# Optimization experiments

Measured on AMD Instinct MI355X. Metric: run time of the kernel, lower is better.

The kernel has to match this reference:

```python
import jax, jax.numpy as jnp
import numpy as np

T, B, A, H = 128, 32, 6, 128  # rollout len, envs, actions, lstm hidden


def _conv(x, w, b, stride):
    # x: NCHW, w: OIHW (torch layout), VALID padding like nn.Conv2d default
    y = jax.lax.conv_general_dilated(
        x, w, (stride, stride), 'VALID',
        dimension_numbers=('NCHW', 'OIHW', 'NCHW'))
    return y + b[None, :, None, None]


def setup_inputs() -> dict:
    key = jax.random.key(0)
    ks = jax.random.split(key, 12)
    s = 0.05  # weight scale to keep activations in a sane range
    inp = {
        'x': jax.random.uniform(ks[0], (T * B, 1, 84, 84), jnp.float32) * 255.0,
        'done': (jax.random.uniform(ks[1], (T * B,)) < 0.05).astype(jnp.float32),
        'h0': jnp.zeros((1, B, H), jnp.float32),
        'c0': jnp.zeros((1, B, H), jnp.float32),
        'W1': jax.random.normal(ks[2], (32, 1, 8, 8), jnp.float32) * s,
        'b1': jnp.zeros((32,), jnp.float32),
        'W2': jax.random.normal(ks[3], (64, 32, 4, 4), jnp.float32) * s,
        'b2': jnp.zeros((64,), jnp.float32),
        'W3': jax.random.normal(ks[4], (64, 64, 3, 3), jnp.float32) * s,
        'b3': jnp.zeros((64,), jnp.float32),
        'Wfc': jax.random.normal(ks[5], (512, 3136), jnp.float32) * s,
        'bfc': jnp.zeros((512,), jnp.float32),
        'W_ih': jax.random.normal(ks[6], (4 * H, 512), jnp.float32) * s,
        'W_hh': jax.random.normal(ks[7], (4 * H, H), jnp.float32) * s,
        'b_ih': jnp.zeros((4 * H,), jnp.float32),
        'b_hh': jnp.zeros((4 * H,), jnp.float32),
        'Wa': jax.random.normal(ks[8], (A, H), jnp.float32) * 0.01,
        'ba': jnp.zeros((A,), jnp.float32),
        'Wc': jax.random.normal(ks[9], (1, H), jnp.float32) * s,
        'bc': jnp.zeros((1,), jnp.float32),
    }
    return inp


def reference(x, done, h0, c0, W1, b1, W2, b2, W3, b3, Wfc, bfc,
              W_ih, W_hh, b_ih, b_hh, Wa, ba, Wc, bc):
    # --- conv feature extractor (x / 255.0) ---
    z = x / 255.0
    z = jax.nn.relu(_conv(z, W1, b1, 4))   # (N,32,20,20)
    z = jax.nn.relu(_conv(z, W2, b2, 2))   # (N,64,9,9)
    z = jax.nn.relu(_conv(z, W3, b3, 1))   # (N,64,7,7)
    z = z.reshape(z.shape[0], -1)           # (N,3136), torch flatten order
    hidden = jax.nn.relu(z @ Wfc.T + bfc)   # (N,512)

    batch = h0.shape[1]
    xs = hidden.reshape(-1, batch, 512)     # (T,B,512)
    ds = done.reshape(-1, batch)            # (T,B)

    # precompute input projection for all steps at once
    gates_x = jnp.einsum('tbi,gi->tbg', xs, W_ih) + b_ih  # (T,B,4H)

    def step(carry, inp):
        h, c = carry
        gx, d = inp
        mask = (1.0 - d)[:, None]           # reset state where done
        h = h * mask
        c = c * mask
        gates = gx + h @ W_hh.T + b_hh
        i, f, g, o = jnp.split(gates, 4, axis=-1)  # torch gate order i,f,g,o
        c = jax.nn.sigmoid(f) * c + jax.nn.sigmoid(i) * jnp.tanh(g)
        h = jax.nn.sigmoid(o) * jnp.tanh(c)
        return (h, c), h

    (hT, cT), hs = jax.lax.scan(step, (h0[0], c0[0]), (gates_x, ds))
    new_hidden = hs.reshape(-1, hs.shape[-1])  # (T*B, 128)

    logits = new_hidden @ Wa.T + ba            # (T*B, A)
    value = new_hidden @ Wc.T + bc             # (T*B, 1)
    return logits, value, hT[None], cT[None]
```

## Files before the change

kernel.cpp:

```cpp
#include <hip/hip_runtime.h>

#define TT 128
#define BB 32
#define NN (TT*BB)

typedef float f4 __attribute__((ext_vector_type(4)));
typedef float f32x4 __attribute__((ext_vector_type(4)));
typedef short s8 __attribute__((ext_vector_type(8)));
typedef short bf16x8 __attribute__((ext_vector_type(8)));
typedef short s4v __attribute__((ext_vector_type(4)));

__device__ __forceinline__ float bf2f(unsigned short u){
  union{unsigned int i; float f;} x; x.i = ((unsigned int)u)<<16; return x.f;
}
__device__ __forceinline__ unsigned short f2bf(float f){
  union{float ff; unsigned int i;} x; x.ff=f;
  unsigned int r = x.i + 0x7FFFu + ((x.i>>16)&1u);
  return (unsigned short)(r>>16);
}
__device__ __forceinline__ float fsig(float x){
  return __builtin_amdgcn_rcpf(1.f + __expf(-x));
}
__device__ __forceinline__ float ftanh(float x){
  return 1.f - 2.f*__builtin_amdgcn_rcpf(1.f + __expf(2.f*x));
}
__device__ __forceinline__ void gload_lds16(const void* g, void* lds){
  __builtin_amdgcn_global_load_lds(
    (const __attribute__((address_space(1))) unsigned int*)g,
    (__attribute__((address_space(3))) unsigned int*)lds, 16, 0, 0);
}

__global__ __launch_bounds__(256) void prep_w1(const float* __restrict__ W1,
    unsigned short* __restrict__ w1c){
  int i = blockIdx.x*256 + threadIdx.x;
  int co = i >> 6; int k = i & 63;
  w1c[i] = (co < 32) ? f2bf(W1[co*64 + k] * (1.f/255.f)) : (unsigned short)0;
}
__global__ __launch_bounds__(256) void prep_w2(const float* __restrict__ W2,
    unsigned short* __restrict__ w2c){
  int i = blockIdx.x*256 + threadIdx.x;
  int co = i >> 9; int rem = i & 511; int khw = rem >> 5; int ci = rem & 31;
  w2c[i] = f2bf(W2[(co*32 + ci)*16 + khw]);
}
__global__ __launch_bounds__(256) void prep_w3(const float* __restrict__ W3,
    unsigned short* __restrict__ w3c){
  int i = blockIdx.x*256 + threadIdx.x;
  int co = i/576; int rem = i - co*576; int khw = rem >> 6; int ci = rem & 63;
  w3c[i] = f2bf(W3[(co*64 + ci)*9 + khw]);
}
__global__ __launch_bounds__(256) void prep_wfc(const float* __restrict__ Wfc,
    unsigned short* __restrict__ wfcc){
  int i = blockIdx.x*256 + threadIdx.x;
  int nn = i/3136; int rem = i - nn*3136; int sp = rem >> 6; int ci = rem & 63;
  wfcc[i] = f2bf(Wfc[nn*3136 + ci*49 + sp]);
}
__global__ __launch_bounds__(256) void prep_wih(const float* __restrict__ W_ih,
    unsigned short* __restrict__ wihc){
  int i = blockIdx.x*256 + threadIdx.x;
  wihc[i] = f2bf(W_ih[i]);
}
__global__ __launch_bounds__(256) void prep_whh(const float* __restrict__ W_hh,
    unsigned short* __restrict__ whhc){
  int i = blockIdx.x*256 + threadIdx.x;
  whhc[i] = f2bf(W_hh[i]);
}
__global__ __launch_bounds__(256) void prep_x(const float* __restrict__ x,
    unsigned short* __restrict__ xb){
  int i = blockIdx.x*256 + threadIdx.x;
  f4 v0 = *(const f4*)(x + (size_t)i*8);
  f4 v1 = *(const f4*)(x + (size_t)i*8 + 4);
  s8 o;
  #pragma unroll
  for(int j=0;j<4;j++){ o[j] = (short)f2bf(v0[j]); o[4+j] = (short)f2bf(v1[j]); }
  *(s8*)&xb[(size_t)i*8] = o;
}

template<int MODE, int OUTBF16, int RELU>
__global__ __launch_bounds__(256) void mgemm_k(
    const unsigned short* __restrict__ A, const unsigned short* __restrict__ B,
    const float* __restrict__ bias1, const float* __restrict__ bias2,
    void* __restrict__ Cout, int K, int Nld, int nout){
  __shared__ unsigned short As[128*40];
  __shared__ unsigned short Bs[64*40];
  int t = threadIdx.x;
  int bm = blockIdx.y, bn = blockIdx.x;
  int arow = t >> 1, ahalf = t & 1;
  int gm = bm*128 + arow;
  const unsigned short* abase;
  if(MODE == 0){
    abase = A + (size_t)gm*K + ahalf*16;
  } else if(MODE == 1){
    int n = gm/81; int r = gm - n*81; int oh = r/9; int ow = r - oh*9;
    abase = A + (((size_t)n*20 + 2*oh)*20 + 2*ow)*32 + ahalf*16;
  } else if(MODE == 2){
    int n = gm/49; int r = gm - n*49; int oh = r/7; int ow = r - oh*7;
    abase = A + (((size_t)n*9 + oh)*9 + ow)*64 + ahalf*16;
  } else {
    int n = gm/400; int r = gm - n*400; int oh = r/20; int ow = r - oh*20;
    abase = A + (size_t)n*7056 + (size_t)(oh*4)*84 + ow*4;
  }
  int brow = t >> 2, bq = t & 3;
  const unsigned short* bbase = B + (size_t)(bn*64 + brow)*K + bq*8;
  int l = t & 63, w = t >> 6;
  int wr = w >> 1, wc = w & 1;
  int lr = l & 15, lk = (l >> 4)*8;
  f32x4 acc[4][2] = {};
  int nsteps = K >> 5;
  for(int s=0; s<nsteps; s++){
    if(MODE == 3){
      const unsigned short* src = abase + (size_t)(s*4 + ahalf*2)*84;
      s4v p0 = *(const s4v*)src;
      s4v p1 = *(const s4v*)(src + 4);
      s4v p2 = *(const s4v*)(src + 84);
      s4v p3 = *(const s4v*)(src + 88);
      *(s4v*)&As[arow*40 + ahalf*16]      = p0;
      *(s4v*)&As[arow*40 + ahalf*16 + 4]  = p1;
      *(s4v*)&As[arow*40 + ahalf*16 + 8]  = p2;
      *(s4v*)&As[arow*40 + ahalf*16 + 12] = p3;
    } else {
      const unsigned short* src;
      if(MODE == 0){
        src = abase + s*32;
      } else if(MODE == 1){
        int kh = s >> 2, kw = s & 3;
        src = abase + (kh*20 + kw)*32;
      } else {
        int khw = s >> 1; int kh = khw/3; int kw = khw - kh*3;
        src = abase + (kh*9 + kw)*64 + (s & 1)*32;
      }
      bf16x8 a0 = *(const bf16x8*)src;
      bf16x8 a1 = *(const bf16x8*)(src + 8);
      *(bf16x8*)&As[arow*40 + ahalf*16] = a0;
      *(bf16x8*)&As[arow*40 + ahalf*16 + 8] = a1;
    }
    bf16x8 bv = *(const bf16x8*)(bbase + s*32);
    *(bf16x8*)&Bs[brow*40 + bq*8] = bv;
    __syncthreads();
    bf16x8 af[4];
    #pragma unroll
    for(int mf=0; mf<4; mf++)
      af[mf] = *(const bf16x8*)&As[(wr*64 + mf*16 + lr)*40 + lk];
    bf16x8 b0 = *(const bf16x8*)&Bs[(wc*32 + lr)*40 + lk];
    bf16x8 b1 = *(const bf16x8*)&Bs[(wc*32 + 16 + lr)*40 + lk];
    #pragma unroll
    for(int mf=0; mf<4; mf++){
      acc[mf][0] = __builtin_amdgcn_mfma_f32_16x16x32_bf16(af[mf], b0, acc[mf][0], 0, 0, 0);
      acc[mf][1] = __builtin_amdgcn_mfma_f32_16x16x32_bf16(af[mf], b1, acc[mf][1], 0, 0, 0);
    }
    __syncthreads();
  }
  #pragma unroll
  for(int nf=0; nf<2; nf++){
    int gcol = bn*64 + wc*32 + nf*16 + lr;
    if(gcol >= nout) continue;
    float bb = bias1[gcol] + (bias2 ? bias2[gcol] : 0.f);
    #pragma unroll
    for(int mf=0; mf<4; mf++){
      #pragma unroll
      for(int reg=0; reg<4; reg++){
        int grow = bm*128 + wr*64 + mf*16 + (l>>4)*4 + reg;
        float v = acc[mf][nf][reg] + bb;
        if(RELU) v = v>0.f ? v : 0.f;
        if(OUTBF16) ((unsigned short*)Cout)[(size_t)grow*Nld + gcol] = f2bf(v);
        else        ((float*)Cout)[(size_t)grow*Nld + gcol] = v;
      }
    }
  }
}

__global__ __launch_bounds__(512) void lstm_v3_k(
    const float* __restrict__ gx,
    const float* __restrict__ done,
    const float* __restrict__ h0, const float* __restrict__ c0,
    const unsigned short* __restrict__ whhc,
    float* __restrict__ hs, float* __restrict__ out_hT, float* __restrict__ out_cT){
  __shared__ float mask_lds[TT*4];
  __shared__ unsigned short hA[2][4][136];
  __shared__ __align__(16) float gxS[3][4][520];
  __shared__ __align__(16) float gW[8][256];
  int tid = threadIdx.x;
  int B0 = blockIdx.x * 4;
  int w = tid >> 6, l = tid & 63;
  int lr = l & 15, lg = l >> 4;
  int cu = 16*w + (l >> 2);
  int cb = l & 3;
  int drow = w >> 1, dhalf = w & 1;

  bf16x8 wA[4][4];
  #pragma unroll
  for(int g=0; g<4; g++)
    #pragma unroll
    for(int kt=0; kt<4; kt++)
      wA[g][kt] = *(const bf16x8*)&whhc[(size_t)(g*128 + 16*w + lr)*128 + kt*32 + lg*8];

  {
    int tt = tid >> 2, bb = tid & 3;
    mask_lds[tid] = 1.f - done[tt*32 + B0 + bb];
  }
  float cv = c0[(size_t)(B0+cb)*128 + cu];
  float hv0 = h0[(size_t)(B0+cb)*128 + cu];
  float hout = 0.f;
  {
    float m0 = 1.f - done[0*BB + B0 + cb];
    hA[0][cb][cu] = f2bf(hv0 * m0);
  }
  #pragma unroll
  for(int sl=0; sl<2; sl++)
    gload_lds16(gx + ((size_t)(sl*32 + B0 + drow))*512 + dhalf*256 + l*4,
                &gxS[sl][drow][dhalf*256]);
  __syncthreads();

  int slot = 0;
  for(int t=0; t<TT; t++){
    int cur = t & 1;
    {
      int ts = (t+2 < TT) ? t+2 : TT-1;
      int s2 = (slot >= 1) ? slot-1 : 2;
      gload_lds16(gx + ((size_t)(ts*32 + B0 + drow))*512 + dhalf*256 + l*4,
                  &gxS[s2][drow][dhalf*256]);
    }
    bf16x8 hF[4];
    #pragma unroll
    for(int kt=0; kt<4; kt++)
      hF[kt] = *(const bf16x8*)&hA[cur][lr & 3][kt*32 + lg*8];
    f32x4 acc[4] = {};
    #pragma unroll
    for(int kt=0; kt<4; kt++)
      #pragma unroll
      for(int g=0; g<4; g++)
        acc[g] = __builtin_amdgcn_mfma_f32_16x16x32_bf16(wA[g][kt], hF[kt], acc[g], 0, 0, 0);
    if(lr < 4){
      #pragma unroll
      for(int g=0; g<4; g++)
        #pragma unroll
        for(int r=0; r<4; r++)
          gW[w][(lg*4 + r)*16 + lr*4 + g] = acc[g][r];
    }
    asm volatile("s_waitcnt lgkmcnt(0)" ::: "memory");
    f4 g4 = *(const f4*)&gW[w][l*4];
    float gx0 = gxS[slot][cb][      cu];
    float gx1 = gxS[slot][cb][128 + cu];
    float gx2 = gxS[slot][cb][256 + cu];
    float gx3 = gxS[slot][cb][384 + cu];
    float m  = mask_lds[t*4 + cb];
    float mn = (t < TT-1) ? mask_lds[(t+1)*4 + cb] : 1.f;
    float iv = fsig (g4[0] + gx0);
    float fv = fsig (g4[1] + gx1);
    float gv = ftanh(g4[2] + gx2);
    float ov = fsig (g4[3] + gx3);
    float cn = fv*(cv*m) + iv*gv;
    float hn = ov*ftanh(cn);
    cv = cn; hout = hn;
    hs[((size_t)t*BB + B0 + cb)*128 + cu] = hn;
    hA[cur^1][cb][cu] = f2bf(hn * mn);
    asm volatile("s_waitcnt vmcnt(3) lgkmcnt(0)" ::: "memory");
    __builtin_amdgcn_s_barrier();
    slot = (slot >= 2) ? 0 : slot+1;
  }
  out_hT[(size_t)(B0+cb)*128 + cu] = hout;
  out_cT[(size_t)(B0+cb)*128 + cu] = cv;
}

__global__ __launch_bounds__(256) void heads_k(const float* __restrict__ hs,
    const float* __restrict__ Wa, const float* __restrict__ ba,
    const float* __restrict__ Wc, const float* __restrict__ bc,
    float* __restrict__ out){
  int gid = blockIdx.x*256 + threadIdx.x;
  int n = gid/7, a = gid - n*7;
  const float* w = (a<6) ? (Wa + a*128) : Wc;
  float bias = (a<6) ? ba[a] : bc[0];
  const float* h = hs + (size_t)n*128;
  float acc = 0.f;
  #pragma unroll
  for(int k=0;k<32;k++){
    f4 hv = *(const f4*)(h + k*4);
    f4 wv = *(const f4*)(w + k*4);
    acc += hv[0]*wv[0]+hv[1]*wv[1]+hv[2]*wv[2]+hv[3]*wv[3];
  }
  float v = acc + bias;
  if(a<6) out[(size_t)n*6 + a] = v;
  else    out[24576 + n] = v;
}

extern "C" void kernel_launch(void* const* d_in, const int* in_sizes, int n_in,
                              void* d_out, int out_size, void* d_ws, size_t ws_size,
                              hipStream_t stream){
  const float* x    = (const float*)d_in[0];
  const float* done = (const float*)d_in[1];
  const float* h0   = (const float*)d_in[2];
  const float* c0   = (const float*)d_in[3];
  const float* W1   = (const float*)d_in[4];
  const float* b1   = (const float*)d_in[5];
  const float* W2   = (const float*)d_in[6];
  const float* b2   = (const float*)d_in[7];
  const float* W3   = (const float*)d_in[8];
  const float* b3   = (const float*)d_in[9];
  const float* Wfc  = (const float*)d_in[10];
  const float* bfc  = (const float*)d_in[11];
  const float* W_ih = (const float*)d_in[12];
  const float* W_hh = (const float*)d_in[13];
  const float* b_ih = (const float*)d_in[14];
  const float* b_hh = (const float*)d_in[15];
  const float* Wa   = (const float*)d_in[16];
  const float* ba   = (const float*)d_in[17];
  const float* Wc   = (const float*)d_in[18];
  const float* bc   = (const float*)d_in[19];
  float* out = (float*)d_out;

  char* ws = (char*)d_ws;
  unsigned short* z1   = (unsigned short*)(ws + 0);
  unsigned short* xb16 = (unsigned short*)(ws + 104857600);
  unsigned short* z2   = (unsigned short*)(ws + 104857600);
  unsigned short* z3   = (unsigned short*)(ws + 0);
  unsigned short* hid  = (unsigned short*)(ws + 25690112);
  float* gx            = (float*)(ws + 29884416);
  float* hs            = (float*)(ws + 38273024);
  unsigned short* w2c  = (unsigned short*)(ws + 162660352);
  unsigned short* w3c  = (unsigned short*)(ws + 162725888);
  unsigned short* wfcc = (unsigned short*)(ws + 162799616);
  unsigned short* wihc = (unsigned short*)(ws + 166010880);
  unsigned short* w1c  = (unsigned short*)(ws + 166535168);
  unsigned short* whhc = (unsigned short*)(ws + 166543360);

  prep_w1 <<<16,  256, 0, stream>>>(W1, w1c);
  prep_w2 <<<128, 256, 0, stream>>>(W2, w2c);
  prep_w3 <<<144, 256, 0, stream>>>(W3, w3c);
  prep_wfc<<<6272,256, 0, stream>>>(Wfc, wfcc);
  prep_wih<<<1024,256, 0, stream>>>(W_ih, wihc);
  prep_whh<<<256, 256, 0, stream>>>(W_hh, whhc);
  prep_x  <<<14112,256,0, stream>>>(x, xb16);

  mgemm_k<3,1,1><<<dim3(1,12800),256,0,stream>>>(xb16, w1c, b1, nullptr, z1, 64, 32, 32);
  mgemm_k<1,1,1><<<dim3(1,2592),256,0,stream>>>(z1, w2c, b2, nullptr, z2, 512, 64, 64);
  mgemm_k<2,1,1><<<dim3(1,1568),256,0,stream>>>(z2, w3c, b3, nullptr, z3, 576, 64, 64);
  mgemm_k<0,1,1><<<dim3(8,32),256,0,stream>>>(z3, wfcc, bfc, nullptr, hid, 3136, 512, 512);
  mgemm_k<0,0,0><<<dim3(8,32),256,0,stream>>>(hid, wihc, b_ih, b_hh, gx, 512, 512, 512);

  lstm_v3_k<<<8,512,0,stream>>>(gx, done, h0, c0, whhc, hs, out+28672, out+32768);
  heads_k<<<112,256,0,stream>>>(hs, Wa, ba, Wc, bc, out);
}
```

Before: 360.2 us.

## Fuse input conversion, conv1 and conv2 into one per-image LDS kernel

Adds a per-image kernel that loads the fp32 frame, converts it to bf16 in LDS, runs conv1 with MFMA into an LDS buffer, then runs conv2 from LDS and writes only z2. This drops the bf16 copy of x, the global z1 round trip and two launches. The conv3 GEMM also gets a block-index swizzle, and the LSTM gate scratch layout changes to scalar reads. One block per image uses a lot of LDS, which can limit occupancy.

```diff
diff --git a/kernel.cpp b/kernel.cpp
--- a/kernel.cpp
+++ b/kernel.cpp
@@ -33,8 +33,7 @@
 __global__ __launch_bounds__(256) void prep_w1(const float* __restrict__ W1,
     unsigned short* __restrict__ w1c){
   int i = blockIdx.x*256 + threadIdx.x;
-  int co = i >> 6; int k = i & 63;
-  w1c[i] = (co < 32) ? f2bf(W1[co*64 + k] * (1.f/255.f)) : (unsigned short)0;
+  w1c[i] = f2bf(W1[i] * (1.f/255.f));
 }
 __global__ __launch_bounds__(256) void prep_w2(const float* __restrict__ W2,
     unsigned short* __restrict__ w2c){
@@ -64,18 +63,114 @@
   int i = blockIdx.x*256 + threadIdx.x;
   whhc[i] = f2bf(W_hh[i]);
 }
-__global__ __launch_bounds__(256) void prep_x(const float* __restrict__ x,
-    unsigned short* __restrict__ xb){
-  int i = blockIdx.x*256 + threadIdx.x;
-  f4 v0 = *(const f4*)(x + (size_t)i*8);
-  f4 v1 = *(const f4*)(x + (size_t)i*8 + 4);
-  s8 o;
-  #pragma unroll
-  for(int j=0;j<4;j++){ o[j] = (short)f2bf(v0[j]); o[4+j] = (short)f2bf(v1[j]); }
-  *(s8*)&xb[(size_t)i*8] = o;
-}
-
-template<int MODE, int OUTBF16, int RELU>
+
+__global__ __launch_bounds__(256) void conv12_k(
+    const float* __restrict__ x,
+    const unsigned short* __restrict__ w1c, const float* __restrict__ b1,
+    const unsigned short* __restrict__ w2c, const float* __restrict__ b2,
+    unsigned short* __restrict__ z2){
+  __shared__ unsigned short xI[84*88];
+  __shared__ unsigned short z1[400*34];
+  __shared__ unsigned short w1L[32*68];
+  __shared__ unsigned short w2L[64*520];
+  int t = threadIdx.x;
+  int n = blockIdx.x;
+  int w = t >> 6, l = t & 63;
+  int lr = l & 15, lg = l >> 4;
+
+  {
+    bf16x8 v = *(const bf16x8*)&w1c[t*8];
+    *(bf16x8*)&w1L[(t>>3)*68 + (t&7)*8] = v;
+  }
+  {
+    int row = t >> 2, c0 = (t & 3)*128;
+    #pragma unroll
+    for(int j=0;j<16;j++){
+      bf16x8 v = *(const bf16x8*)&w2c[row*512 + c0 + j*8];
+      *(bf16x8*)&w2L[row*520 + c0 + j*8] = v;
+    }
+  }
+  {
+    const float* xb = x + (size_t)n*7056;
+    #pragma unroll
+    for(int j=0;j<7;j++){
+      int idx = t + 256*j;
+      if(idx < 1764){
+        f4 v = *(const f4*)(xb + idx*4);
+        s4v p;
+        #pragma unroll
+        for(int e=0;e<4;e++) p[e] = (short)f2bf(v[e]);
+        int row = idx/21, col = (idx - row*21)*4;
+        *(s4v*)&xI[row*88 + col] = p;
+      }
+    }
+  }
+  __syncthreads();
+
+  bf16x8 bf1[2][2];
+  #pragma unroll
+  for(int nt=0;nt<2;nt++)
+    #pragma unroll
+    for(int s=0;s<2;s++)
+      bf1[nt][s] = *(const bf16x8*)&w1L[(nt*16+lr)*68 + s*32 + lg*8];
+  for(int mt=w; mt<25; mt+=4){
+    int p = mt*16 + lr;
+    int oh = p/20, ow = p - oh*20;
+    bf16x8 a0 = *(const bf16x8*)&xI[(oh*4 + lg    )*88 + ow*4];
+    bf16x8 a1 = *(const bf16x8*)&xI[(oh*4 + 4 + lg)*88 + ow*4];
+    f32x4 acc[2] = {};
+    acc[0] = __builtin_amdgcn_mfma_f32_16x16x32_bf16(a0, bf1[0][0], acc[0], 0,0,0);
+    acc[0] = __builtin_amdgcn_mfma_f32_16x16x32_bf16(a1, bf1[0][1], acc[0], 0,0,0);
+    acc[1] = __builtin_amdgcn_mfma_f32_16x16x32_bf16(a0, bf1[1][0], acc[1], 0,0,0);
+    acc[1] = __builtin_amdgcn_mfma_f32_16x16x32_bf16(a1, bf1[1][1], acc[1], 0,0,0);
+    #pragma unroll
+    for(int nt=0;nt<2;nt++){
+      int ch = nt*16 + lr;
+      float bb = b1[ch];
+      #pragma unroll
+      for(int reg=0;reg<4;reg++){
+        int pp = mt*16 + lg*4 + reg;
+        float v = acc[nt][reg] + bb; v = v>0.f ? v : 0.f;
+        z1[pp*34 + ch] = f2bf(v);
+      }
+    }
+  }
+  __syncthreads();
+
+  int rbase[6];
+  #pragma unroll
+  for(int mt=0;mt<6;mt++){
+    int q = mt*16 + lr; if(q > 80) q = 80;
+    int oh = q/9, ow = q - oh*9;
+    rbase[mt] = (2*oh)*20 + 2*ow;
+  }
+  f32x4 acc2[6] = {};
+  for(int s=0;s<16;s++){
+    int kh = s>>2, kw = s&3;
+    bf16x8 bfr = *(const bf16x8*)&w2L[(w*16+lr)*520 + s*32 + lg*8];
+    #pragma unroll
+    for(int mt=0;mt<6;mt++){
+      bf16x8 af = *(const bf16x8*)&z1[(rbase[mt] + kh*20 + kw)*34 + lg*8];
+      acc2[mt] = __builtin_amdgcn_mfma_f32_16x16x32_bf16(af, bfr, acc2[mt], 0,0,0);
+    }
+  }
+  {
+    int ch = w*16 + lr;
+    float bb = b2[ch];
+    #pragma unroll
+    for(int mt=0;mt<6;mt++)
+      #pragma unroll
+      for(int reg=0;reg<4;reg++){
+        int q = mt*16 + lg*4 + reg;
+        if(q < 81){
+          float v = acc2[mt][reg] + bb; v = v>0.f ? v : 0.f;
+          z2[((size_t)n*81 + q)*64 + ch] = f2bf(v);
+        }
+      }
+  }
+}
+
+template<int MODE, int OUTBF16, int RELU, int SWZ>
 __global__ __launch_bounds__(256) void mgemm_k(
     const unsigned short* __restrict__ A, const unsigned short* __restrict__ B,
     const float* __restrict__ bias1, const float* __restrict__ bias2,
@@ -84,20 +179,18 @@
   __shared__ unsigned short Bs[64*40];
   int t = threadIdx.x;
   int bm = blockIdx.y, bn = blockIdx.x;
+  if(SWZ){
+    int cpx = gridDim.y >> 3;
+    bm = (bm & 7)*cpx + (bm >> 3);
+  }
   int arow = t >> 1, ahalf = t & 1;
   int gm = bm*128 + arow;
   const unsigned short* abase;
   if(MODE == 0){
     abase = A + (size_t)gm*K + ahalf*16;
-  } else if(MODE == 1){
-    int n = gm/81; int r = gm - n*81; int oh = r/9; int ow = r - oh*9;
-    abase = A + (((size_t)n*20 + 2*oh)*20 + 2*ow)*32 + ahalf*16;
-  } else if(MODE == 2){
+  } else {
     int n = gm/49; int r = gm - n*49; int oh = r/7; int ow = r - oh*7;
     abase = A + (((size_t)n*9 + oh)*9 + ow)*64 + ahalf*16;
-  } else {
-    int n = gm/400; int r = gm - n*400; int oh = r/20; int ow = r - oh*20;
-    abase = A + (size_t)n*7056 + (size_t)(oh*4)*84 + ow*4;
   }
   int brow = t >> 2, bq = t & 3;
   const unsigned short* bbase = B + (size_t)(bn*64 + brow)*K + bq*8;
@@ -107,32 +200,17 @@
   f32x4 acc[4][2] = {};
   int nsteps = K >> 5;
   for(int s=0; s<nsteps; s++){
-    if(MODE == 3){
-      const unsigned short* src = abase + (size_t)(s*4 + ahalf*2)*84;
-      s4v p0 = *(const s4v*)src;
-      s4v p1 = *(const s4v*)(src + 4);
-      s4v p2 = *(const s4v*)(src + 84);
-      s4v p3 = *(const s4v*)(src + 88);
-      *(s4v*)&As[arow*40 + ahalf*16]      = p0;
-      *(s4v*)&As[arow*40 + ahalf*16 + 4]  = p1;
-      *(s4v*)&As[arow*40 + ahalf*16 + 8]  = p2;
-      *(s4v*)&As[arow*40 + ahalf*16 + 12] = p3;
+    const unsigned short* src;
+    if(MODE == 0){
+      src = abase + s*32;
     } else {
-      const unsigned short* src;
-      if(MODE == 0){
-        src = abase + s*32;
-      } else if(MODE == 1){
-        int kh = s >> 2, kw = s & 3;
-        src = abase + (kh*20 + kw)*32;
-      } else {
-        int khw = s >> 1; int kh = khw/3; int kw = khw - kh*3;
-        src = abase + (kh*9 + kw)*64 + (s & 1)*32;
-      }
-      bf16x8 a0 = *(const bf16x8*)src;
-      bf16x8 a1 = *(const bf16x8*)(src + 8);
-      *(bf16x8*)&As[arow*40 + ahalf*16] = a0;
-      *(bf16x8*)&As[arow*40 + ahalf*16 + 8] = a1;
-    }
+      int khw = s >> 1; int kh = khw/3; int kw = khw - kh*3;
+      src = abase + (kh*9 + kw)*64 + (s & 1)*32;
+    }
+    bf16x8 a0 = *(const bf16x8*)src;
+    bf16x8 a1 = *(const bf16x8*)(src + 8);
+    *(bf16x8*)&As[arow*40 + ahalf*16] = a0;
+    *(bf16x8*)&As[arow*40 + ahalf*16 + 8] = a1;
     bf16x8 bv = *(const bf16x8*)(bbase + s*32);
     *(bf16x8*)&Bs[brow*40 + bq*8] = bv;
     __syncthreads();
@@ -234,20 +312,23 @@
       for(int g=0; g<4; g++)
         #pragma unroll
         for(int r=0; r<4; r++)
-          gW[w][(lg*4 + r)*16 + lr*4 + g] = acc[g][r];
+          gW[w][g*64 + (lg*4 + r)*4 + lr] = acc[g][r];
     }
     asm volatile("s_waitcnt lgkmcnt(0)" ::: "memory");
-    f4 g4 = *(const f4*)&gW[w][l*4];
+    float g0 = gW[w][      l];
+    float g1 = gW[w][ 64 + l];
+    float g2 = gW[w][128 + l];
+    float g3 = gW[w][192 + l];
     float gx0 = gxS[slot][cb][      cu];
     float gx1 = gxS[slot][cb][128 + cu];
     float gx2 = gxS[slot][cb][256 + cu];
     float gx3 = gxS[slot][cb][384 + cu];
     float m  = mask_lds[t*4 + cb];
     float mn = (t < TT-1) ? mask_lds[(t+1)*4 + cb] : 1.f;
-    float iv = fsig (g4[0] + gx0);
-    float fv = fsig (g4[1] + gx1);
-    float gv = ftanh(g4[2] + gx2);
-    float ov = fsig (g4[3] + gx3);
+    float iv = fsig (g0 + gx0);
+    float fv = fsig (g1 + gx1);
+    float gv = ftanh(g2 + gx2);
+    float ov = fsig (g3 + gx3);
     float cn = fv*(cv*m) + iv*gv;
     float hn = ov*ftanh(cn);
     cv = cn; hout = hn;
@@ -308,33 +389,29 @@
   float* out = (float*)d_out;
 
   char* ws = (char*)d_ws;
-  unsigned short* z1   = (unsigned short*)(ws + 0);
-  unsigned short* xb16 = (unsigned short*)(ws + 104857600);
-  unsigned short* z2   = (unsigned short*)(ws + 104857600);
-  unsigned short* z3   = (unsigned short*)(ws + 0);
-  unsigned short* hid  = (unsigned short*)(ws + 25690112);
-  float* gx            = (float*)(ws + 29884416);
-  float* hs            = (float*)(ws + 38273024);
-  unsigned short* w2c  = (unsigned short*)(ws + 162660352);
-  unsigned short* w3c  = (unsigned short*)(ws + 162725888);
-  unsigned short* wfcc = (unsigned short*)(ws + 162799616);
-  unsigned short* wihc = (unsigned short*)(ws + 166010880);
-  unsigned short* w1c  = (unsigned short*)(ws + 166535168);
-  unsigned short* whhc = (unsigned short*)(ws + 166543360);
-
-  prep_w1 <<<16,  256, 0, stream>>>(W1, w1c);
+  unsigned short* z2   = (unsigned short*)(ws + 0);
+  unsigned short* z3   = (unsigned short*)(ws + 42467328);
+  unsigned short* hid  = (unsigned short*)(ws + 68157440);
+  float* gx            = (float*)(ws + 72351744);
+  float* hs            = (float*)(ws + 80740352);
+  unsigned short* w1c  = (unsigned short*)(ws + 82837504);
+  unsigned short* w2c  = (unsigned short*)(ws + 82845696);
+  unsigned short* w3c  = (unsigned short*)(ws + 82911232);
+  unsigned short* wfcc = (unsigned short*)(ws + 82984960);
+  unsigned short* wihc = (unsigned short*)(ws + 86196224);
+  unsigned short* whhc = (unsigned short*)(ws + 86720512);
+
+  prep_w1 <<<8,   256, 0, stream>>>(W1, w1c);
   prep_w2 <<<128, 256, 0, stream>>>(W2, w2c);
   prep_w3 <<<144, 256, 0, stream>>>(W3, w3c);
   prep_wfc<<<6272,256, 0, stream>>>(Wfc, wfcc);
   prep_wih<<<1024,256, 0, stream>>>(W_ih, wihc);
   prep_whh<<<256, 256, 0, stream>>>(W_hh, whhc);
-  prep_x  <<<14112,256,0, stream>>>(x, xb16);
-
-  mgemm_k<3,1,1><<<dim3(1,12800),256,0,stream>>>(xb16, w1c, b1, nullptr, z1, 64, 32, 32);
-  mgemm_k<1,1,1><<<dim3(1,2592),256,0,stream>>>(z1, w2c, b2, nullptr, z2, 512, 64, 64);
-  mgemm_k<2,1,1><<<dim3(1,1568),256,0,stream>>>(z2, w3c, b3, nullptr, z3, 576, 64, 64);
-  mgemm_k<0,1,1><<<dim3(8,32),256,0,stream>>>(z3, wfcc, bfc, nullptr, hid, 3136, 512, 512);
-  mgemm_k<0,0,0><<<dim3(8,32),256,0,stream>>>(hid, wihc, b_ih, b_hh, gx, 512, 512, 512);
+
+  conv12_k<<<4096,256,0,stream>>>(x, w1c, b1, w2c, b2, z2);
+  mgemm_k<2,1,1,1><<<dim3(1,1568),256,0,stream>>>(z2, w3c, b3, nullptr, z3, 576, 64, 64);
+  mgemm_k<0,1,1,0><<<dim3(8,32),256,0,stream>>>(z3, wfcc, bfc, nullptr, hid, 3136, 512, 512);
+  mgemm_k<0,0,0,0><<<dim3(8,32),256,0,stream>>>(hid, wihc, b_ih, b_hh, gx, 512, 512, 512);
 
   lstm_v3_k<<<8,512,0,stream>>>(gx, done, h0, c0, whhc, hs, out+28672, out+32768);
   heads_k<<<112,256,0,stream>>>(hs, Wa, ba, Wc, bc, out);
```

Measured after the change: 416.1 us. +15.5%, slower.
